# Kernel optimization log

Measured on AMD Instinct MI355X. Metric: run time of the kernel, lower is better.

The kernel has to match this reference:

```python
import jax, jax.numpy as jnp
import numpy as np

L = 524288      # input_length (~33 s @ 16 kHz)
C = 129         # cochlear channels
DS = 80         # downsample rate = sr / (1000 / frame_length)


def setup_inputs() -> dict:
    key = jax.random.key(0)
    k0, k1, k2 = jax.random.split(key, 3)
    x = jax.random.normal(k0, (L,), dtype=jnp.float32)
    # Filterbank transfer functions (stand-in for cochlear_filter_params.npz)
    Hs_real = 0.1 * jax.random.normal(k1, (C, L), dtype=jnp.float32)
    Hs_imag = 0.1 * jax.random.normal(k2, (C, L), dtype=jnp.float32)
    alpha_comp = jnp.full((C,), 0.9, dtype=jnp.float32)
    alpha_leak = jnp.array(0.9922179, dtype=jnp.float32)
    li_kernel = jnp.array([1.0, -1.0], dtype=jnp.float32)  # first-difference conv kernel
    return {"x": x, "Hs_real": Hs_real, "Hs_imag": Hs_imag,
            "alpha_comp": alpha_comp, "alpha_leak": alpha_leak,
            "li_kernel": li_kernel}


def reference(x, Hs_real, Hs_imag, alpha_comp, alpha_leak, li_kernel):
    # 1. Cochlear filterbank: FFT -> per-channel complex multiply -> IFFT
    X = jnp.fft.fft(x)                                   # [L] complex
    Hs = Hs_real + 1j * Hs_imag                          # [C, L]
    coch = jnp.fft.ifft(Hs * X[None, :], axis=-1).real   # [C, L]

    # 2. Power-law compression per channel: |x|^a * sign(x)
    comp = jnp.abs(coch) ** alpha_comp[:, None] * jnp.sign(coch)

    # 3-4. LIN: first difference along channel axis (SAME pad -> zero row at end), then ReLU
    shifted = jnp.concatenate([comp[1:], jnp.zeros_like(comp[:1])], axis=0)
    lin = jax.nn.relu(comp * li_kernel[0] + shifted * li_kernel[1])

    # 5. Leaky integration via FFT-domain filtering, then downsample
    freqs = jnp.fft.fftfreq(L).astype(jnp.float32) * (2.0 * jnp.pi)
    Hleak = 1.0 / (1.0 - alpha_leak * (jnp.cos(freqs) - 1j * jnp.sin(freqs)))  # [L]
    out = jnp.fft.ifft(Hleak[None, :] * jnp.fft.fft(lin, axis=-1), axis=-1).real
    return out[:, DS - 1::DS]                            # [C, L // DS]
```

## Files before the change

### kernel.cpp

```cpp
#include <hip/hip_runtime.h>
#include <math.h>

#define LN    524288
#define N1    512
#define N2    1024
#define NCH   129
#define DSR   80
#define NOUT  6553
#define OB2   64
#define NBLK  103
#define SPB   (OB2*DSR)
#define TPW   20
#define NPAIR 65
#define KTAIL 48
#define SB    1024
#define LMAP(i) ((i) + ((i) >> 3))
#define SWZ(p)  ((p) ^ ((((p) >> 5) & 1) * 31))

__device__ __forceinline__ float2 cmulf(float2 a, float2 b) {
    return make_float2(a.x*b.x - a.y*b.y, a.x*b.y + a.y*b.x);
}

__device__ __forceinline__ float powsign(float x, float a) {
    float m = __builtin_amdgcn_exp2f(a * __builtin_amdgcn_logf(fabsf(x)));
    return copysignf(m, x);
}

__global__ void pack_x(const float* __restrict__ x, float2* __restrict__ dst) {
    int i = blockIdx.x * 256 + threadIdx.x;
    dst[i] = make_float2(x[i], 0.f);
}

__global__ void transpose_c(const float2* __restrict__ src, float2* __restrict__ dst,
                            int R, int Cc) {
    __shared__ float2 tile[32][33];
    size_t boff = (size_t)blockIdx.z * LN;
    src += boff; dst += boff;
    int x  = blockIdx.x * 32 + threadIdx.x;
    int y0 = blockIdx.y * 32 + threadIdx.y;
#pragma unroll
    for (int i = 0; i < 32; i += 8)
        tile[threadIdx.y + i][threadIdx.x] = src[(size_t)(y0 + i) * Cc + x];
    __syncthreads();
    int xo  = blockIdx.y * 32 + threadIdx.x;
    int yo0 = blockIdx.x * 32 + threadIdx.y;
#pragma unroll
    for (int i = 0; i < 32; i += 8)
        dst[(size_t)(yo0 + i) * R + xo] = tile[threadIdx.x][threadIdx.y + i];
}

template<int M, int SIGN, int TW>
__global__ __launch_bounds__(256) void fft_rows(const float2* __restrict__ src,
                                                float2* __restrict__ dst,
                                                int rows_per_batch) {
    __shared__ __align__(16) float2 ping[M];
    __shared__ __align__(16) float2 pong[M];
    __shared__ float2 twid[M];
    size_t rowg = blockIdx.x;
    const float2* srow = src + rowg * M;
    float2* drow = dst + rowg * M;
    int row = (int)(rowg % (size_t)rows_per_batch);
    int t = threadIdx.x;
    const float4* s4 = (const float4*)srow;
    for (int ii = t; ii < M/2; ii += 256)
        *(float4*)&ping[2*ii] = s4[ii];
    for (int i = t; i < M; i += 256) {
        if (i >= 1) {
            int h = 1 << (31 - __clz((unsigned)i));
            float ang = (float)SIGN * 3.14159265358979323846f * (float)(i - h) / (float)h;
            float s, c; __sincosf(ang, &s, &c);
            twid[i] = make_float2(c, s);
        }
    }
    __syncthreads();
    float2* a = ping;
    float2* b = pong;
    for (int Ns = 1; Ns < M; Ns <<= 1) {
        for (int j = t; j < M/2; j += 256) {
            int jm = j & (Ns - 1);
            float2 v0 = a[j];
            float2 v1 = a[j + M/2];
            float2 tw = twid[Ns + jm];
            float2 w = make_float2(v1.x*tw.x - v1.y*tw.y, v1.x*tw.y + v1.y*tw.x);
            int d0 = ((j & ~(Ns - 1)) << 1) | jm;
            b[d0]      = make_float2(v0.x + w.x, v0.y + w.y);
            b[d0 + Ns] = make_float2(v0.x - w.x, v0.y - w.y);
        }
        __syncthreads();
        float2* tmp = a; a = b; b = tmp;
    }
    if (TW) {
        const float c2pi = 6.28318530717958647692f / (float)LN;
        for (int i = t; i < M; i += 256) {
            float2 v = a[i];
            unsigned prod = ((unsigned)row * (unsigned)i) & (unsigned)(LN - 1);
            float ang = (float)SIGN * c2pi * (float)prod;
            float s, c;
            __sincosf(ang, &s, &c);
            drow[i] = make_float2(v.x*c - v.y*s, v.x*s + v.y*c);
        }
    } else {
        float4* d4 = (float4*)drow;
        for (int ii = t; ii < M/2; ii += 256)
            d4[ii] = *(const float4*)&a[2*ii];
    }
}

__device__ __forceinline__ void herm2(float2 X1,
                                      float har,  float hai,  float hbr,  float hbi,
                                      float har2, float hai2, float hbr2, float hbi2,
                                      bool hasB, float2& Wk, float2& WkL) {
    float2 a1 = make_float2(har*X1.x - hai*X1.y, har*X1.y + hai*X1.x);
    float2 a2 = make_float2(har2*X1.x + hai2*X1.y, hai2*X1.x - har2*X1.y);
    float yar = 0.5f*(a1.x + a2.x), yai = 0.5f*(a1.y - a2.y);
    float ybr = 0.f, ybi = 0.f;
    if (hasB) {
        float2 b1 = make_float2(hbr*X1.x - hbi*X1.y, hbr*X1.y + hbi*X1.x);
        float2 b2 = make_float2(hbr2*X1.x + hbi2*X1.y, hbi2*X1.x - hbr2*X1.y);
        ybr = 0.5f*(b1.x + b2.x); ybi = 0.5f*(b1.y - b2.y);
    }
    Wk  = make_float2(yar - ybi, yai + ybr);
    WkL = make_float2(yar + ybi, ybr - yai);
}

__global__ __launch_bounds__(256) void build_w6(const float* __restrict__ Hr,
                                                const float* __restrict__ Hi,
                                                const float2* __restrict__ X,
                                                float2* __restrict__ W, int pair0) {
    __shared__ float mirS[4][1160];
    int s0 = blockIdx.x * SB;
    int pl = blockIdx.y;
    int p  = pair0 + pl;
    int ca = 2*p, cb = 2*p + 1;
    bool hasB = (cb < NCH);
    const float* Hs0 = Hr + (size_t)ca * LN;
    const float* Hs1 = Hi + (size_t)ca * LN;
    const float* Hs2 = hasB ? (Hr + (size_t)cb * LN) : Hs0;
    const float* Hs3 = hasB ? (Hi + (size_t)cb * LN) : Hs1;
    const float* Hs[4] = {Hs0, Hs1, Hs2, Hs3};
    float2* Wp = W + (size_t)pl * LN;
    int t = threadIdx.x;
    int j4 = 4 * t;
    int mbase = LN - s0 - SB;

    float4 lowv[4];
#pragma unroll
    for (int a = 0; a < 4; a++) {
        lowv[a] = *(const float4*)&Hs[a][s0 + j4];
        float4 mv = *(const float4*)&Hs[a][mbase + j4];
        int lm = LMAP(j4);
        mirS[a][lm+0] = mv.x; mirS[a][lm+1] = mv.y; mirS[a][lm+2] = mv.z; mirS[a][lm+3] = mv.w;
    }
    if (t == 1 && s0 > 0) {
#pragma unroll
        for (int a = 0; a < 4; a++) mirS[a][LMAP(SB)] = Hs[a][LN - s0];
    }
    float nxt[4];
#pragma unroll
    for (int a = 0; a < 4; a++) nxt[a] = __shfl_down(lowv[a].x, 1);
    if ((t & 63) == 63) {
#pragma unroll
        for (int a = 0; a < 4; a++) nxt[a] = Hs[a][s0 + j4 + 4];
    }
    __syncthreads();

    float4 xa = *(const float4*)&X[s0 + j4];
    float4 xb = *(const float4*)&X[s0 + j4 + 2];
    float2 wlo[4];
#pragma unroll
    for (int d = 0; d < 4; d++) {
        int k = s0 + j4 + d;
        float2 Xk = (d == 0) ? make_float2(xa.x, xa.y) :
                    (d == 1) ? make_float2(xa.z, xa.w) :
                    (d == 2) ? make_float2(xb.x, xb.y) : make_float2(xb.z, xb.w);
        float hl[4] = { (d==0)?lowv[0].x:(d==1)?lowv[0].y:(d==2)?lowv[0].z:lowv[0].w,
                        (d==0)?lowv[1].x:(d==1)?lowv[1].y:(d==2)?lowv[1].z:lowv[1].w,
                        (d==0)?lowv[2].x:(d==1)?lowv[2].y:(d==2)?lowv[2].z:lowv[2].w,
                        (d==0)?lowv[3].x:(d==1)?lowv[3].y:(d==2)?lowv[3].z:lowv[3].w };
        if (k == 0) {
            float2 Ya = cmulf(make_float2(hl[0], hl[1]), Xk);
            float br = 0.f;
            if (hasB) { float2 Yb = cmulf(make_float2(hl[2], hl[3]), Xk); br = Yb.x; }
            wlo[d] = make_float2(Ya.x, br);
        } else {
            int jm = LMAP(SB - j4 - d);
            float2 Wk, WkL;
            herm2(Xk, hl[0], hl[1], hl[2], hl[3],
                      mirS[0][jm], mirS[1][jm], mirS[2][jm], mirS[3][jm], hasB, Wk, WkL);
            wlo[d] = Wk;
        }
    }
    *(float4*)&Wp[s0 + j4]     = make_float4(wlo[0].x, wlo[0].y, wlo[1].x, wlo[1].y);
    *(float4*)&Wp[s0 + j4 + 2] = make_float4(wlo[2].x, wlo[2].y, wlo[3].x, wlo[3].y);

    int e0 = SB - 4 - j4;
    float2 wmi[4];
#pragma unroll
    for (int d = 0; d < 4; d++) {
        int ee = e0 + d;
        int m  = mbase + ee;
        int jm = LMAP(ee);
        if (m == LN/2) {
            float2 Xv = X[LN/2];
            float2 Ya = cmulf(make_float2(mirS[0][jm], mirS[1][jm]), Xv);
            float br = 0.f;
            if (hasB) { float2 Yb = cmulf(make_float2(mirS[2][jm], mirS[3][jm]), Xv); br = Yb.x; }
            wmi[d] = make_float2(Ya.x, br);
        } else {
            int kp = LN - m;
            float hl[4];
#pragma unroll
            for (int a = 0; a < 4; a++)
                hl[a] = (d==0) ? nxt[a] : (d==1) ? lowv[a].w : (d==2) ? lowv[a].z : lowv[a].y;
            float2 Xk = X[kp];
            float2 Wk, WkL;
            herm2(Xk, hl[0], hl[1], hl[2], hl[3],
                      mirS[0][jm], mirS[1][jm], mirS[2][jm], mirS[3][jm], hasB, Wk, WkL);
            wmi[d] = WkL;
        }
    }
    *(float4*)&Wp[mbase + e0]     = make_float4(wmi[0].x, wmi[0].y, wmi[1].x, wmi[1].y);
    *(float4*)&Wp[mbase + e0 + 2] = make_float4(wmi[2].x, wmi[2].y, wmi[3].x, wmi[3].y);
}

__global__ __launch_bounds__(1024) void kB(float2* __restrict__ D1) {
    __shared__ float sRe[16][545];
    __shared__ float sIm[16][545];
    __shared__ float2 twid[512];
    int cg = blockIdx.x;
    int pl = blockIdx.y;
    float2* Dp = D1 + (size_t)pl * LN;
    unsigned c_base = 16u * cg;
    int t = threadIdx.x;

    if (t >= 1 && t < 512) {
        int h = 1 << (31 - __clz((unsigned)t));
        float ang = 3.14159265358979323846f * (float)(t - h) / (float)h;
        float s, c; __sincosf(ang, &s, &c);
        twid[t] = make_float2(c, s);
    }

    int cc = t & 15;
    int g  = (t >> 4) & 3;
    int w  = t >> 6;

#pragma unroll
    for (int i = 0; i < 8; i++) {
        int r = w + (g << 4) + (i << 6);
        float2 v = Dp[(size_t)r * N2 + c_base + cc];
        int sp = SWZ(r);
        sRe[cc][sp] = v.x;
        sIm[cc][sp] = v.y;
    }
    __syncthreads();

    int cc2 = t >> 6;
    int l   = t & 63;
    for (int h = 256; h >= 1; h >>= 1) {
#pragma unroll
        for (int i = 0; i < 4; i++) {
            int j = l + (i << 6);
            int q = j & (h - 1);
            int base = ((j & ~(h - 1)) << 1) | q;
            float2 tw = twid[h + q];
            int p0 = SWZ(base), p1 = SWZ(base + h);
            float are = sRe[cc2][p0], aim = sIm[cc2][p0];
            float bre = sRe[cc2][p1], bim = sIm[cc2][p1];
            sRe[cc2][p0] = are + bre;  sIm[cc2][p0] = aim + bim;
            float dre = are - bre, dim = aim - bim;
            sRe[cc2][p1] = dre*tw.x - dim*tw.y;
            sIm[cc2][p1] = dre*tw.y + dim*tw.x;
        }
        __syncthreads();
    }

    const float c2pi = 6.28318530717958647692f / (float)LN;
    unsigned truec = c_base + (unsigned)cc;
#pragma unroll
    for (int i = 0; i < 8; i++) {
        int pos = w + (g << 4) + (i << 6);
        unsigned jj = __brev((unsigned)pos) >> 23;
        int sp = SWZ(pos);
        float re = sRe[cc][sp], im = sIm[cc][sp];
        unsigned prod = (jj * truec) & (unsigned)(LN - 1);
        float ang = c2pi * (float)prod;
        float s, c;
        __sincosf(ang, &s, &c);
        Dp[(size_t)jj * N2 + truec] = make_float2(re*c - im*s, re*s + im*c);
    }
}

__global__ __launch_bounds__(256) void ifft_finish(const float2* __restrict__ src,
                                                   float* __restrict__ comp,
                                                   const float* __restrict__ alpha_comp,
                                                   int pair0) {
    __shared__ __align__(16) float2 tile[32][33];
    int pl = blockIdx.z;
    int p = pair0 + pl;
    int ca = 2*p, cb = 2*p + 1;
    const float2* s = src + (size_t)pl * LN;
    int m0 = blockIdx.x * 32, j0 = blockIdx.y * 32;
    int tx = threadIdx.x, ty = threadIdx.y;
    int tid = ty * 8 + tx;
    int jl = tid >> 3, mq = tid & 7;
    const float4* row4 = (const float4*)&s[(size_t)(j0 + jl) * N2 + m0 + mq * 4];
    float4 a = row4[0], b = row4[1];
    tile[jl][mq*4+0] = make_float2(a.x, a.y);
    tile[jl][mq*4+1] = make_float2(a.z, a.w);
    tile[jl][mq*4+2] = make_float2(b.x, b.y);
    tile[jl][mq*4+3] = make_float2(b.z, b.w);
    __syncthreads();
    float aa = alpha_comp[ca];
    float ab = (cb < NCH) ? alpha_comp[cb] : 1.f;
    const float invL = 1.f / (float)LN;
    float oa[4], ob[4];
#pragma unroll
    for (int d = 0; d < 4; d++) {
        float2 v = tile[4*tx + d][ty];
        oa[d] = powsign(v.x * invL, aa);
        ob[d] = powsign(v.y * invL, ab);
    }
    size_t n0 = (size_t)(m0 + ty) * N1 + j0 + 4*tx;
    *(float4*)&comp[(size_t)ca * LN + n0] = make_float4(oa[0], oa[1], oa[2], oa[3]);
    if (cb < NCH)
        *(float4*)&comp[(size_t)cb * LN + n0] = make_float4(ob[0], ob[1], ob[2], ob[3]);
}

__global__ __launch_bounds__(256) void iir_part1(
    const float* __restrict__ comp, const float* __restrict__ alpha_leak,
    const float* __restrict__ li_kernel, float* __restrict__ out,
    float* __restrict__ carryOut) {
    __shared__ float win[SPB + SPB/TPW];
    __shared__ float wv[4], wg[4];
    int blk = blockIdx.x;
    int c = blockIdx.y;
    int t = threadIdx.x;
    float alpha = alpha_leak[0];
    float k0 = li_kernel[0], k1 = li_kernel[1];
    int base = blk * SPB;
    const int cap = NOUT * DSR;
    const float* c0 = comp + (size_t)c * LN;
    const float* c1 = (c + 1 < NCH) ? comp + (size_t)(c + 1) * LN : nullptr;
    const float4 z4 = make_float4(0.f, 0.f, 0.f, 0.f);
    for (int i4 = 4*t; i4 < SPB; i4 += 1024) {
        int g = base + i4;
        float4 u0 = *(const float4*)&c0[g];
        float4 u1 = c1 ? *(const float4*)&c1[g] : z4;
        float vv[4] = {k0*u0.x + k1*u1.x, k0*u0.y + k1*u1.y,
                       k0*u0.z + k1*u1.z, k0*u0.w + k1*u1.w};
#pragma unroll
        for (int d = 0; d < 4; d++) {
            float v = fmaxf(vv[d], 0.f);
            if (g + d >= cap) v = 0.f;
            int i = i4 + d;
            win[i + i / TPW] = v;
        }
    }
    __syncthreads();
    float v = 0.f;
    int lbase = 21 * t;
#pragma unroll
    for (int i = 0; i < TPW; i++)
        v = fmaf(alpha, v, win[lbase + i]);
    float g = powf(alpha, (float)TPW);
    int lid = t & 63, wid = t >> 6;
#pragma unroll
    for (int d = 1; d < 64; d <<= 1) {
        float pv = __shfl_up(v, d);
        float pg = __shfl_up(g, d);
        if (lid >= d) { v = fmaf(g, pv, v); g = g * pg; }
    }
    if (lid == 63) { wv[wid] = v; wg[wid] = g; }
    __syncthreads();
    float cv = 0.f;
#pragma unroll
    for (int w = 0; w < 3; w++)
        if (w < wid) cv = wv[w] + wg[w] * cv;
    float vf = fmaf(g, cv, v);
    int nact = NOUT - blk * OB2; if (nact > OB2) nact = OB2;
    if ((t & 3) == 3) {
        int o = t >> 2;
        if (o < nact)
            out[(size_t)c * NOUT + blk * OB2 + o] = vf;
    }
    if (t == 4 * nact - 1)
        carryOut[c * NBLK + blk] = vf;
}

__global__ void iir_part2(const float* __restrict__ comp, const float* __restrict__ alpha_leak,
                          const float* __restrict__ li_kernel,
                          const float* __restrict__ carryOut, float* __restrict__ D) {
    int c = threadIdx.x;
    if (c >= NCH) return;
    float alpha = alpha_leak[0];
    float k0 = li_kernel[0], k1 = li_kernel[1];
    const float* c0 = comp + (size_t)c * LN;
    const float* c1 = (c + 1 < NCH) ? comp + (size_t)(c + 1) * LN : nullptr;
    float tail = 0.f, ap = 1.f;
    for (int j = 0; j < KTAIL; j++) {
        int g = LN - 1 - j;
        float u0 = c0[g];
        float u1 = c1 ? c1[g] : 0.f;
        float v = k0 * u0 + k1 * u1; v = v > 0.f ? v : 0.f;
        tail += ap * v;
        ap *= alpha;
    }
    float D0 = tail + ap * carryOut[c * NBLK + (NBLK - 1)]
             + powf(alpha, (float)(KTAIL + 2000)) * carryOut[c * NBLK + (NBLK - 2)];
    D[c * NBLK + 0] = D0;
    for (int b = 1; b < NBLK; b++)
        D[c * NBLK + b] = carryOut[c * NBLK + b - 1];
}

__global__ void iir_part3(const float* __restrict__ D, const float* __restrict__ alpha_leak,
                          float* __restrict__ out) {
    int idx = blockIdx.x * 256 + threadIdx.x;
    if (idx >= NCH * NOUT) return;
    int c = idx / NOUT, m = idx - c * NOUT;
    int b = m / OB2, o = m - b * OB2;
    float alpha = alpha_leak[0];
    float beta = powf(alpha, (float)DSR);
    float dec = powf(beta, (float)(o + 1));
    out[idx] += dec * D[c * NBLK + b];
}

extern "C" void kernel_launch(void* const* d_in, const int* in_sizes, int n_in,
                              void* d_out, int out_size, void* d_ws, size_t ws_size,
                              hipStream_t stream) {
    const float* x  = (const float*)d_in[0];
    const float* Hr = (const float*)d_in[1];
    const float* Hi = (const float*)d_in[2];
    const float* ac = (const float*)d_in[3];
    const float* al = (const float*)d_in[4];
    const float* li = (const float*)d_in[5];
    float* out = (float*)d_out;

    char* ws = (char*)d_ws;
    size_t off = 0;
    auto alloc = [&](size_t bytes) -> void* {
        void* p = ws + off;
        off += (bytes + 255) & ~(size_t)255;
        return p;
    };
    float2* Xf     = (float2*)alloc((size_t)LN * sizeof(float2));
    float*  comp   = (float*) alloc((size_t)NCH * LN * sizeof(float));
    float*  cOut   = (float*) alloc((size_t)NCH * NBLK * sizeof(float));
    float*  Dbuf   = (float*) alloc((size_t)NCH * NBLK * sizeof(float));
    size_t remain = (ws_size > off) ? (ws_size - off) : 0;
    int chunk = (int)(remain / ((size_t)LN * sizeof(float2)));
    if (chunk > NPAIR) chunk = NPAIR;
    if (chunk < 2)     chunk = 2;
    float2* bufA = (float2*)alloc((size_t)chunk * LN * sizeof(float2));

    dim3 tb(32, 8, 1);

    float2* fA = bufA;
    float2* fB = bufA + LN;
    pack_x<<<LN / 256, 256, 0, stream>>>(x, fA);
    transpose_c<<<dim3(N2/32, N1/32, 1), tb, 0, stream>>>(fA, fB, N1, N2);
    fft_rows<N1, -1, 1><<<N2, 256, 0, stream>>>(fB, fB, N2);
    transpose_c<<<dim3(N1/32, N2/32, 1), tb, 0, stream>>>(fB, fA, N2, N1);
    fft_rows<N2, -1, 0><<<N1, 256, 0, stream>>>(fA, fA, N1);
    transpose_c<<<dim3(N2/32, N1/32, 1), tb, 0, stream>>>(fA, Xf, N1, N2);

    for (int ci = 0; ci < NPAIR; ci += chunk) {
        int np = NPAIR - ci; if (np > chunk) np = chunk;
        build_w6<<<dim3(LN/2/SB, np), 256, 0, stream>>>(Hr, Hi, Xf, bufA, ci);
        kB<<<dim3(64, np), 1024, 0, stream>>>(bufA);
        fft_rows<N2, 1, 0><<<N1 * np, 256, 0, stream>>>(bufA, bufA, N1);
        ifft_finish<<<dim3(32, 16, np), dim3(8, 32), 0, stream>>>(bufA, comp, ac, ci);
    }

    iir_part1<<<dim3(NBLK, NCH, 1), 256, 0, stream>>>(comp, al, li, out, cOut);
    iir_part2<<<1, 256, 0, stream>>>(comp, al, li, cOut, Dbuf);
    iir_part3<<<(NCH * NOUT + 255) / 256, 256, 0, stream>>>(Dbuf, al, out);
}
```

Baseline: 669.3 us.

## Fuse final inverse FFT stage with transpose and power-law compression

Replaces the separate row-FFT pass and transpose/compression kernel with one kernel. Each block loads 8 rows of 1024 complex values into swizzled shared memory and runs a radix-2 DIF FFT with on-chip twiddles. It then writes the bit-reversed, compressed results straight into the channel-major comp buffer. This removes one full global read/write round trip of the intermediate buffer and a kernel launch. The cost is scalar strided stores in place of float4 stores, plus ten synchronised radix-2 passes.

Result: no change. 656.2 us (-2.0%).

```diff
diff --git a/kernel.cpp b/kernel.cpp
--- a/kernel.cpp
+++ b/kernel.cpp
@@ -290,40 +290,76 @@
     }
 }
 
-__global__ __launch_bounds__(256) void ifft_finish(const float2* __restrict__ src,
-                                                   float* __restrict__ comp,
-                                                   const float* __restrict__ alpha_comp,
-                                                   int pair0) {
-    __shared__ __align__(16) float2 tile[32][33];
-    int pl = blockIdx.z;
-    int p = pair0 + pl;
+__global__ __launch_bounds__(512) void kC(const float2* __restrict__ D1,
+                                          float* __restrict__ comp,
+                                          const float* __restrict__ alpha_comp,
+                                          int pair0) {
+    __shared__ float sRe[8][1057];
+    __shared__ float sIm[8][1057];
+    __shared__ float2 twid[1024];
+    int rg = blockIdx.x;
+    int pl = blockIdx.y;
+    int p  = pair0 + pl;
     int ca = 2*p, cb = 2*p + 1;
-    const float2* s = src + (size_t)pl * LN;
-    int m0 = blockIdx.x * 32, j0 = blockIdx.y * 32;
-    int tx = threadIdx.x, ty = threadIdx.y;
-    int tid = ty * 8 + tx;
-    int jl = tid >> 3, mq = tid & 7;
-    const float4* row4 = (const float4*)&s[(size_t)(j0 + jl) * N2 + m0 + mq * 4];
-    float4 a = row4[0], b = row4[1];
-    tile[jl][mq*4+0] = make_float2(a.x, a.y);
-    tile[jl][mq*4+1] = make_float2(a.z, a.w);
-    tile[jl][mq*4+2] = make_float2(b.x, b.y);
-    tile[jl][mq*4+3] = make_float2(b.z, b.w);
-    __syncthreads();
+    const float2* Dp = D1 + (size_t)pl * LN;
+    int jj0 = rg * 8;
+    int t = threadIdx.x;
+    for (int i = t; i < 1024; i += 512) {
+        if (i >= 1) {
+            int h = 1 << (31 - __clz((unsigned)i));
+            float ang = 3.14159265358979323846f * (float)(i - h) / (float)h;
+            float s, c; __sincosf(ang, &s, &c);
+            twid[i] = make_float2(c, s);
+        }
+    }
+    int w = t >> 6, l = t & 63;
+
+    const float4* rowp = (const float4*)(Dp + (size_t)(jj0 + w) * N2);
+#pragma unroll
+    for (int i = 0; i < 8; i++) {
+        int q4 = l + (i << 6);
+        float4 v = rowp[q4];
+        int a0 = SWZ(2*q4), a1 = SWZ(2*q4 + 1);
+        sRe[w][a0] = v.x; sIm[w][a0] = v.y;
+        sRe[w][a1] = v.z; sIm[w][a1] = v.w;
+    }
+    __syncthreads();
+
+    for (int h = 512; h >= 1; h >>= 1) {
+#pragma unroll
+        for (int i = 0; i < 8; i++) {
+            int j = l + (i << 6);
+            int q = j & (h - 1);
+            int base = ((j & ~(h - 1)) << 1) | q;
+            float2 tw = twid[h + q];
+            int p0 = SWZ(base), p1 = SWZ(base + h);
+            float are = sRe[w][p0], aim = sIm[w][p0];
+            float bre = sRe[w][p1], bim = sIm[w][p1];
+            sRe[w][p0] = are + bre;  sIm[w][p0] = aim + bim;
+            float dre = are - bre, dim = aim - bim;
+            sRe[w][p1] = dre*tw.x - dim*tw.y;
+            sIm[w][p1] = dre*tw.y + dim*tw.x;
+        }
+        __syncthreads();
+    }
+
     float aa = alpha_comp[ca];
     float ab = (cb < NCH) ? alpha_comp[cb] : 1.f;
     const float invL = 1.f / (float)LN;
-    float oa[4], ob[4];
-#pragma unroll
-    for (int d = 0; d < 4; d++) {
-        float2 v = tile[4*tx + d][ty];
-        oa[d] = powsign(v.x * invL, aa);
-        ob[d] = powsign(v.y * invL, ab);
-    }
-    size_t n0 = (size_t)(m0 + ty) * N1 + j0 + 4*tx;
-    *(float4*)&comp[(size_t)ca * LN + n0] = make_float4(oa[0], oa[1], oa[2], oa[3]);
-    if (cb < NCH)
-        *(float4*)&comp[(size_t)cb * LN + n0] = make_float4(ob[0], ob[1], ob[2], ob[3]);
+    int r  = t & 7;
+    int dm = (t >> 3) & 7;
+#pragma unroll
+    for (int i = 0; i < 16; i++) {
+        int m = (w << 7) + (i << 3) + dm;
+        unsigned pp = __brev((unsigned)m) >> 22;
+        int sp = SWZ((int)pp);
+        float re = sRe[r][sp] * invL;
+        float im = sIm[r][sp] * invL;
+        size_t n = (size_t)m * N1 + jj0 + r;
+        comp[(size_t)ca * LN + n] = powsign(re, aa);
+        if (cb < NCH)
+            comp[(size_t)cb * LN + n] = powsign(im, ab);
+    }
 }
 
 __global__ __launch_bounds__(256) void iir_part1(
@@ -467,8 +503,7 @@
         int np = NPAIR - ci; if (np > chunk) np = chunk;
         build_w6<<<dim3(LN/2/SB, np), 256, 0, stream>>>(Hr, Hi, Xf, bufA, ci);
         kB<<<dim3(64, np), 1024, 0, stream>>>(bufA);
-        fft_rows<N2, 1, 0><<<N1 * np, 256, 0, stream>>>(bufA, bufA, N1);
-        ifft_finish<<<dim3(32, 16, np), dim3(8, 32), 0, stream>>>(bufA, comp, ac, ci);
+        kC<<<dim3(64, np), 512, 0, stream>>>(bufA, comp, ac, ci);
     }
 
     iir_part1<<<dim3(NBLK, NCH, 1), 256, 0, stream>>>(comp, al, li, out, cOut);
```
